# Performance work log

Measured on AMD Instinct MI355X. Metric: run time of the kernel, lower is better.

The kernel has to match this reference:

```python
import jax, jax.numpy as jnp
import numpy as np

BATCH = 32
NUM_VARS = 16
SAMPLES = 4096
EMBED_DIM = 128
WINDOW_SIZE = 32
STEP_SIZE = 4
WIDTH = 1.0


def setup_inputs() -> dict:
    key = jax.random.key(0)
    k1, k2, k3, k4, k5 = jax.random.split(key, 5)
    x = jax.random.normal(k1, (BATCH, NUM_VARS, SAMPLES), dtype=jnp.float32)
    # sample-level LSH: num_variables -> embed_dim
    W_sample = jax.random.normal(k2, (NUM_VARS, EMBED_DIM), dtype=jnp.float32)
    b_sample = jax.random.uniform(k3, (EMBED_DIM,), dtype=jnp.float32, minval=0.0, maxval=WIDTH)
    # patch-level LSH: window_size*embed_dim -> embed_dim
    W_patch = jax.random.normal(k4, (WINDOW_SIZE * EMBED_DIM, EMBED_DIM), dtype=jnp.float32)
    b_patch = jax.random.uniform(k5, (EMBED_DIM,), dtype=jnp.float32, minval=0.0, maxval=WIDTH)
    return {"x": x, "W_sample": W_sample, "b_sample": b_sample,
            "W_patch": W_patch, "b_patch": b_patch}


def reference(x, W_sample, b_sample, W_patch, b_patch):
    batch, v, samples = x.shape
    # encode: E2LSH hash of every timestep, fully vectorized over the samples axis
    # enc: [B, S, D]
    enc = jnp.floor((jnp.einsum('bvs,vd->bsd', x, W_sample) + b_sample) / WIDTH)
    # quantize: sliding windows over time, flattened then hashed
    num_tokens = (samples - WINDOW_SIZE) // STEP_SIZE  # matches preallocated tokens
    # idx: [T, W] gather indices for all windows at once
    idx = jnp.arange(num_tokens)[:, None] * STEP_SIZE + jnp.arange(WINDOW_SIZE)[None, :]
    windows = enc[:, idx, :].reshape(batch, num_tokens, WINDOW_SIZE * EMBED_DIM)  # [B, T, W*D]
    tokens = jnp.floor((windows @ W_patch + b_patch) / WIDTH)  # [B, T, D]
    return tokens
```

## Files before the change

### kernel.cpp

```cpp
#include <hip/hip_runtime.h>
#include <hip/hip_bf16.h>
#include <cstdint>

#define BATCH   32
#define NVARS   16
#define SAMPLES 4096
#define EDIM    128
#define NTOK    1016
#define PLELEM  4368

typedef __bf16 bf8_t __attribute__((ext_vector_type(8)));
typedef float  f4_t  __attribute__((ext_vector_type(4)));

__global__ __launch_bounds__(256) void prep_kernel(
    const float* __restrict__ Wp, __hip_bfloat16* __restrict__ WtF)
{
  __shared__ float ls[32][132];
  int tid = threadIdx.x;
  int kb  = blockIdx.x;
  int s = kb >> 3, dlt = kb & 7;
  int kbase = (4 * dlt + (s & 3)) * 128 + (s >> 2) * 32;
#pragma unroll
  for (int r = 0; r < 16; ++r) {
    int idx = tid + r * 256;
    ls[idx >> 7][idx & 127] =
        Wp[(size_t)(kbase + (idx >> 7)) * EDIM + (idx & 127)];
  }
  __syncthreads();
  int g = tid >> 5, l5 = tid & 31;
#pragma unroll
  for (int h = 0; h < 2; ++h) {
    int lane = l5 + h * 32;
    int quad = lane >> 4, l15 = lane & 15;
    int n = g * 16 + l15;
    union { unsigned short u[8]; uint4 v; } pk;
#pragma unroll
    for (int t = 0; t < 8; ++t) {
      __hip_bfloat16 hh = __float2bfloat16(ls[quad * 8 + t][n]);
      pk.u[t] = *(unsigned short*)&hh;
    }
    *(uint4*)(WtF + (size_t)kb * 4096 + g * 512 + lane * 8) = pk.v;
  }
}

__global__ __launch_bounds__(512, 1) void fused_kernel(
    const float* __restrict__ x,
    const float* __restrict__ Ws,
    const float* __restrict__ bs,
    const __hip_bfloat16* __restrict__ WtF,
    const float* __restrict__ bp,
    float* __restrict__ out)
{
  __shared__ __align__(16) __hip_bfloat16 Apan[16 * PLELEM];
  __shared__ __align__(16) float xTp[2][136][16];

  int tid  = threadIdx.x;
  int lane = tid & 63;
  int wv   = tid >> 6;
  int g2   = wv >> 1;
  int nh   = wv & 1;
  int b    = blockIdx.x >> 3;
  int t0   = (blockIdx.x & 7) << 7;
  int quad = lane >> 4;
  int l15  = lane & 15;

  const __hip_bfloat16* bg = WtF + (size_t)(nh * 4) * 512 + lane * 8;

  int q4 = tid & 31;
  int eq = q4 >> 3;
  int cq = (q4 >> 1) & 3;
  int hq = q4 & 1;
  int r0 = tid >> 5;

  float w[NVARS][4];
  float bz[4];
  {
    int d0 = q4 * 4;
#pragma unroll
    for (int v = 0; v < NVARS; ++v)
      *(float4*)&w[v][0] = *(const float4*)(Ws + v * EDIM + d0);
    *(float4*)&bz[0] = *(const float4*)(bs + d0);
  }

  int vv = tid & 15, rr = tid >> 4;
  float4 xreg[5];
  {
    const float* xb = x + ((size_t)b * NVARS + vv) * SAMPLES;
#pragma unroll
    for (int j = 0; j < 4; ++j) {
      int s4 = (t0 + rr + 32 * j) * 4;
      xreg[j] = *(const float4*)(xb + s4);
    }
    if (tid < 128) {
      int s4 = (t0 + 128 + rr) * 4;
      if (s4 > SAMPLES - 4) s4 = SAMPLES - 4;
      xreg[4] = *(const float4*)(xb + s4);
    }
  }

  auto stageX = [&](int p, int buf) {
#pragma unroll
    for (int j = 0; j < 4; ++j) {
      float c = (p == 0) ? xreg[j].x : (p == 1) ? xreg[j].y
              : (p == 2) ? xreg[j].z : xreg[j].w;
      xTp[buf][rr + 32 * j][vv] = c;
    }
    if (tid < 128) {
      float c = (p == 0) ? xreg[4].x : (p == 1) ? xreg[4].y
              : (p == 2) ? xreg[4].z : xreg[4].w;
      xTp[buf][128 + rr][vv] = c;
    }
  };

  auto encTask = [&](int p, int buf, int r) {
    const float* xr = &xTp[buf][r][0];
    float xv[NVARS];
    *(float4*)&xv[0]  = *(const float4*)(xr + 0);
    *(float4*)&xv[4]  = *(const float4*)(xr + 4);
    *(float4*)&xv[8]  = *(const float4*)(xr + 8);
    *(float4*)&xv[12] = *(const float4*)(xr + 12);
    float a0 = bz[0], a1 = bz[1], a2 = bz[2], a3 = bz[3];
#pragma unroll
    for (int v = 0; v < NVARS; ++v) {
      a0 += xv[v] * w[v][0]; a1 += xv[v] * w[v][1];
      a2 += xv[v] * w[v][2]; a3 += xv[v] * w[v][3];
    }
    union { unsigned short us[4]; uint2 q; } pk;
    pk.us[0] = (unsigned short)(__float_as_uint(floorf(a0)) >> 16);
    pk.us[1] = (unsigned short)(__float_as_uint(floorf(a1)) >> 16);
    pk.us[2] = (unsigned short)(__float_as_uint(floorf(a2)) >> 16);
    pk.us[3] = (unsigned short)(__float_as_uint(floorf(a3)) >> 16);
    int phys = (cq + (r >> 1)) & 3;
    char* plbase = (char*)&Apan[(eq * 4 + p) * PLELEM];
    *(uint2*)(plbase + r * 64 + phys * 16 + hq * 8) = pk.q;
  };

  stageX(0, 0);
  __syncthreads();
#pragma unroll
  for (int p = 0; p < 4; ++p) {
    if (p < 3) stageX(p + 1, (p + 1) & 1);
    int buf = p & 1;
#pragma unroll
    for (int j = 0; j < 8; ++j) encTask(p, buf, r0 + 16 * j);
    if (tid < 256) encTask(p, buf, 128 + (tid >> 5));
    __syncthreads();
  }

  f4_t acc[8][4];
  f4_t zero = {0.f, 0.f, 0.f, 0.f};
#pragma unroll
  for (int i = 0; i < 8; ++i)
#pragma unroll
    for (int j = 0; j < 4; ++j) acc[i][j] = zero;

  auto loadB = [&](int kb, uint4* d) {
#pragma unroll
    for (int j = 0; j < 4; ++j)
      d[j] = *(const uint4*)(bg + (size_t)kb * 4096 + j * 512);
  };

  auto loadAF = [&](bf8_t* af, const bf8_t* pA, int dlt) {
    int swz = (quad + ((t0 + dlt + l15) >> 1)) & 3;
#pragma unroll
    for (int i = 0; i < 8; ++i)
      af[i] = pA[(dlt + i * 16 + l15) * 4 + swz];
  };

  auto mstep = [&](const bf8_t* af, const uint4* bq_) {
    __builtin_amdgcn_s_setprio(1);
#pragma unroll
    for (int mi = 0; mi < 8; ++mi)
#pragma unroll
      for (int ni = 0; ni < 4; ++ni)
        acc[mi][ni] = __builtin_amdgcn_mfma_f32_16x16x32_bf16(
            af[mi], __builtin_bit_cast(bf8_t, bq_[ni]), acc[mi][ni], 0, 0, 0);
    __builtin_amdgcn_s_setprio(0);
  };

  bf8_t afA[8], afB[8];
  uint4 bq[2][4];
  loadB(g2 * 32 + 0, bq[0]);
  loadB(g2 * 32 + 1, bq[1]);
  loadAF(afA, (const bf8_t*)&Apan[(g2 * 4) * PLELEM], 0);

  for (int ss = 0; ss < 4; ++ss) {
    const bf8_t* pA  = (const bf8_t*)&Apan[(g2 * 4 + ss) * PLELEM];
    const bf8_t* pAn = (const bf8_t*)&Apan[(g2 * 4 + ss + 1) * PLELEM];
#pragma unroll
    for (int d = 0; d < 8; ++d) {
      int kl = ss * 8 + d;
      if ((d & 1) == 0) {
        if (d < 7) loadAF(afB, pA, d + 1);
        mstep(afA, bq[0]);
      } else {
        if (d < 7)      loadAF(afA, pA, d + 1);
        else if (ss < 3) loadAF(afA, pAn, 0);
        mstep(afB, bq[1]);
      }
      if (kl < 30) loadB(g2 * 32 + kl + 2, bq[d & 1]);
    }
  }

  float* rb2 = (float*)&Apan[0];
  float bias[4];
#pragma unroll
  for (int ni = 0; ni < 4; ++ni) bias[ni] = bp[(nh << 6) + ni * 16 + l15];

#pragma unroll
  for (int rd = 0; rd < 4; ++rd) {
    __syncthreads();
    if (g2 > 0) {
      int slot = ((g2 - 1) * 2 + nh) * 64 + lane;
#pragma unroll
      for (int mh = 0; mh < 2; ++mh) {
        int mi = rd * 2 + mh;
#pragma unroll
        for (int ni = 0; ni < 4; ++ni)
          *(f4_t*)&rb2[(size_t)(slot + mh * 384) * 20 + ni * 4] = acc[mi][ni];
      }
    }
    __syncthreads();
    if (g2 == 0) {
#pragma unroll
      for (int mh = 0; mh < 2; ++mh) {
        int mi = rd * 2 + mh;
        f4_t s0 = acc[mi][0], s1 = acc[mi][1];
        f4_t s2 = acc[mi][2], s3 = acc[mi][3];
#pragma unroll
        for (int q = 1; q < 4; ++q) {
          int sl = ((q - 1) * 2 + nh) * 64 + lane + mh * 384;
          s0 += *(const f4_t*)&rb2[(size_t)sl * 20 + 0];
          s1 += *(const f4_t*)&rb2[(size_t)sl * 20 + 4];
          s2 += *(const f4_t*)&rb2[(size_t)sl * 20 + 8];
          s3 += *(const f4_t*)&rb2[(size_t)sl * 20 + 12];
        }
        f4_t sv[4] = {s0, s1, s2, s3};
#pragma unroll
        for (int ni = 0; ni < 4; ++ni)
#pragma unroll
          for (int r = 0; r < 4; ++r) {
            int t = t0 + mi * 16 + quad * 4 + r;
            if (t < NTOK) {
              int n = (nh << 6) + ni * 16 + l15;
              out[((size_t)b * NTOK + t) * EDIM + n] =
                  floorf(sv[ni][r] + bias[ni]);
            }
          }
      }
    }
  }
}

extern "C" void kernel_launch(void* const* d_in, const int* in_sizes, int n_in,
                              void* d_out, int out_size, void* d_ws, size_t ws_size,
                              hipStream_t stream) {
  const float* x  = (const float*)d_in[0];
  const float* Ws = (const float*)d_in[1];
  const float* bs = (const float*)d_in[2];
  const float* Wp = (const float*)d_in[3];
  const float* bp = (const float*)d_in[4];
  float* out = (float*)d_out;

  __hip_bfloat16* WtF = (__hip_bfloat16*)d_ws;

  prep_kernel<<<128, 256, 0, stream>>>(Wp, WtF);
  fused_kernel<<<BATCH * 8, 512, 0, stream>>>(x, Ws, bs, WtF, bp, out);
}
```

Before: 110.1 us.

## Double block size to 1024 threads, splitting M tile across wave pairs

```diff
diff --git a/kernel.cpp b/kernel.cpp
--- a/kernel.cpp
+++ b/kernel.cpp
@@ -43,7 +43,7 @@
   }
 }
 
-__global__ __launch_bounds__(512, 1) void fused_kernel(
+__global__ __launch_bounds__(1024) void fused_kernel(
     const float* __restrict__ x,
     const float* __restrict__ Ws,
     const float* __restrict__ bs,
@@ -57,8 +57,9 @@
   int tid  = threadIdx.x;
   int lane = tid & 63;
   int wv   = tid >> 6;
-  int g2   = wv >> 1;
-  int nh   = wv & 1;
+  int g2   = wv >> 2;
+  int nh   = (wv >> 1) & 1;
+  int mh   = wv & 1;
   int b    = blockIdx.x >> 3;
   int t0   = (blockIdx.x & 7) << 7;
   int quad = lane >> 4;
@@ -83,32 +84,29 @@
   }
 
   int vv = tid & 15, rr = tid >> 4;
-  float4 xreg[5];
+  float4 xreg[3];
   {
     const float* xb = x + ((size_t)b * NVARS + vv) * SAMPLES;
-#pragma unroll
-    for (int j = 0; j < 4; ++j) {
-      int s4 = (t0 + rr + 32 * j) * 4;
-      xreg[j] = *(const float4*)(xb + s4);
-    }
+    xreg[0] = *(const float4*)(xb + (t0 + rr) * 4);
+    xreg[1] = *(const float4*)(xb + (t0 + 64 + rr) * 4);
     if (tid < 128) {
       int s4 = (t0 + 128 + rr) * 4;
       if (s4 > SAMPLES - 4) s4 = SAMPLES - 4;
-      xreg[4] = *(const float4*)(xb + s4);
+      xreg[2] = *(const float4*)(xb + s4);
     }
   }
 
   auto stageX = [&](int p, int buf) {
-#pragma unroll
-    for (int j = 0; j < 4; ++j) {
-      float c = (p == 0) ? xreg[j].x : (p == 1) ? xreg[j].y
-              : (p == 2) ? xreg[j].z : xreg[j].w;
-      xTp[buf][rr + 32 * j][vv] = c;
-    }
+    float c0 = (p == 0) ? xreg[0].x : (p == 1) ? xreg[0].y
+             : (p == 2) ? xreg[0].z : xreg[0].w;
+    float c1 = (p == 0) ? xreg[1].x : (p == 1) ? xreg[1].y
+             : (p == 2) ? xreg[1].z : xreg[1].w;
+    xTp[buf][rr][vv]      = c0;
+    xTp[buf][64 + rr][vv] = c1;
     if (tid < 128) {
-      float c = (p == 0) ? xreg[4].x : (p == 1) ? xreg[4].y
-              : (p == 2) ? xreg[4].z : xreg[4].w;
-      xTp[buf][128 + rr][vv] = c;
+      float c2 = (p == 0) ? xreg[2].x : (p == 1) ? xreg[2].y
+               : (p == 2) ? xreg[2].z : xreg[2].w;
+      xTp[buf][128 + rr][vv] = c2;
     }
   };
 
@@ -142,15 +140,15 @@
     if (p < 3) stageX(p + 1, (p + 1) & 1);
     int buf = p & 1;
 #pragma unroll
-    for (int j = 0; j < 8; ++j) encTask(p, buf, r0 + 16 * j);
+    for (int j = 0; j < 4; ++j) encTask(p, buf, r0 + 32 * j);
     if (tid < 256) encTask(p, buf, 128 + (tid >> 5));
     __syncthreads();
   }
 
-  f4_t acc[8][4];
+  f4_t acc[4][4];
   f4_t zero = {0.f, 0.f, 0.f, 0.f};
 #pragma unroll
-  for (int i = 0; i < 8; ++i)
+  for (int i = 0; i < 4; ++i)
 #pragma unroll
     for (int j = 0; j < 4; ++j) acc[i][j] = zero;
 
@@ -161,16 +159,16 @@
   };
 
   auto loadAF = [&](bf8_t* af, const bf8_t* pA, int dlt) {
-    int swz = (quad + ((t0 + dlt + l15) >> 1)) & 3;
-#pragma unroll
-    for (int i = 0; i < 8; ++i)
-      af[i] = pA[(dlt + i * 16 + l15) * 4 + swz];
+    int swz = (quad + ((t0 + mh * 64 + dlt + l15) >> 1)) & 3;
+#pragma unroll
+    for (int i = 0; i < 4; ++i)
+      af[i] = pA[(mh * 64 + dlt + i * 16 + l15) * 4 + swz];
   };
 
   auto mstep = [&](const bf8_t* af, const uint4* bq_) {
     __builtin_amdgcn_s_setprio(1);
 #pragma unroll
-    for (int mi = 0; mi < 8; ++mi)
+    for (int mi = 0; mi < 4; ++mi)
 #pragma unroll
       for (int ni = 0; ni < 4; ++ni)
         acc[mi][ni] = __builtin_amdgcn_mfma_f32_16x16x32_bf16(
@@ -178,31 +176,24 @@
     __builtin_amdgcn_s_setprio(0);
   };
 
-  bf8_t afA[8], afB[8];
+  bf8_t af[4];
   uint4 bq[2][4];
   loadB(g2 * 32 + 0, bq[0]);
   loadB(g2 * 32 + 1, bq[1]);
-  loadAF(afA, (const bf8_t*)&Apan[(g2 * 4) * PLELEM], 0);
 
   for (int ss = 0; ss < 4; ++ss) {
-    const bf8_t* pA  = (const bf8_t*)&Apan[(g2 * 4 + ss) * PLELEM];
-    const bf8_t* pAn = (const bf8_t*)&Apan[(g2 * 4 + ss + 1) * PLELEM];
+    const bf8_t* pA = (const bf8_t*)&Apan[(g2 * 4 + ss) * PLELEM];
 #pragma unroll
     for (int d = 0; d < 8; ++d) {
       int kl = ss * 8 + d;
-      if ((d & 1) == 0) {
-        if (d < 7) loadAF(afB, pA, d + 1);
-        mstep(afA, bq[0]);
-      } else {
-        if (d < 7)      loadAF(afA, pA, d + 1);
-        else if (ss < 3) loadAF(afA, pAn, 0);
-        mstep(afB, bq[1]);
-      }
+      loadAF(af, pA, d);
+      mstep(af, bq[d & 1]);
       if (kl < 30) loadB(g2 * 32 + kl + 2, bq[d & 1]);
     }
   }
 
   float* rb2 = (float*)&Apan[0];
+  int idx4 = nh * 2 + mh;
   float bias[4];
 #pragma unroll
   for (int ni = 0; ni < 4; ++ni) bias[ni] = bp[(nh << 6) + ni * 16 + l15];
@@ -211,43 +202,35 @@
   for (int rd = 0; rd < 4; ++rd) {
     __syncthreads();
     if (g2 > 0) {
-      int slot = ((g2 - 1) * 2 + nh) * 64 + lane;
-#pragma unroll
-      for (int mh = 0; mh < 2; ++mh) {
-        int mi = rd * 2 + mh;
-#pragma unroll
-        for (int ni = 0; ni < 4; ++ni)
-          *(f4_t*)&rb2[(size_t)(slot + mh * 384) * 20 + ni * 4] = acc[mi][ni];
-      }
+      int slot = ((g2 - 1) * 4 + idx4) * 64 + lane;
+#pragma unroll
+      for (int ni = 0; ni < 4; ++ni)
+        *(f4_t*)&rb2[(size_t)slot * 20 + ni * 4] = acc[rd][ni];
     }
     __syncthreads();
     if (g2 == 0) {
-#pragma unroll
-      for (int mh = 0; mh < 2; ++mh) {
-        int mi = rd * 2 + mh;
-        f4_t s0 = acc[mi][0], s1 = acc[mi][1];
-        f4_t s2 = acc[mi][2], s3 = acc[mi][3];
-#pragma unroll
-        for (int q = 1; q < 4; ++q) {
-          int sl = ((q - 1) * 2 + nh) * 64 + lane + mh * 384;
-          s0 += *(const f4_t*)&rb2[(size_t)sl * 20 + 0];
-          s1 += *(const f4_t*)&rb2[(size_t)sl * 20 + 4];
-          s2 += *(const f4_t*)&rb2[(size_t)sl * 20 + 8];
-          s3 += *(const f4_t*)&rb2[(size_t)sl * 20 + 12];
+      f4_t s0 = acc[rd][0], s1 = acc[rd][1];
+      f4_t s2 = acc[rd][2], s3 = acc[rd][3];
+#pragma unroll
+      for (int q = 1; q < 4; ++q) {
+        int sl = ((q - 1) * 4 + idx4) * 64 + lane;
+        s0 += *(const f4_t*)&rb2[(size_t)sl * 20 + 0];
+        s1 += *(const f4_t*)&rb2[(size_t)sl * 20 + 4];
+        s2 += *(const f4_t*)&rb2[(size_t)sl * 20 + 8];
+        s3 += *(const f4_t*)&rb2[(size_t)sl * 20 + 12];
+      }
+      f4_t sv[4] = {s0, s1, s2, s3};
+#pragma unroll
+      for (int ni = 0; ni < 4; ++ni)
+#pragma unroll
+        for (int r = 0; r < 4; ++r) {
+          int t = t0 + mh * 64 + rd * 16 + quad * 4 + r;
+          if (t < NTOK) {
+            int n = (nh << 6) + ni * 16 + l15;
+            out[((size_t)b * NTOK + t) * EDIM + n] =
+                floorf(sv[ni][r] + bias[ni]);
+          }
         }
-        f4_t sv[4] = {s0, s1, s2, s3};
-#pragma unroll
-        for (int ni = 0; ni < 4; ++ni)
-#pragma unroll
-          for (int r = 0; r < 4; ++r) {
-            int t = t0 + mi * 16 + quad * 4 + r;
-            if (t < NTOK) {
-              int n = (nh << 6) + ni * 16 + l15;
-              out[((size_t)b * NTOK + t) * EDIM + n] =
-                  floorf(sv[ni][r] + bias[ni]);
-            }
-          }
-      }
     }
   }
 }
@@ -265,5 +248,5 @@
   __hip_bfloat16* WtF = (__hip_bfloat16*)d_ws;
 
   prep_kernel<<<128, 256, 0, stream>>>(Wp, WtF);
-  fused_kernel<<<BATCH * 8, 512, 0, stream>>>(x, Ws, bs, WtF, bp, out);
+  fused_kernel<<<BATCH * 8, 1024, 0, stream>>>(x, Ws, bs, WtF, bp, out);
 }
```

Measured after the change: 123.9 us. 12.5% more time.
